# Optimization experiments

Measured on AMD Instinct MI355X. Metric: run time of the kernel, lower is better.

Reference implementation:

```python
import jax, jax.numpy as jnp
import numpy as np

KERNEL = 9


def setup_inputs() -> dict:
    key = jax.random.key(0)
    k1, k2 = jax.random.split(key)
    n, c, h, w = 1, 256, 256, 256
    key_feature = jax.random.normal(k1, (n, c, h, w), dtype=jnp.float32)
    weights = jax.random.normal(k2, (1, KERNEL * KERNEL, h, w), dtype=jnp.float32)
    return {"key_feature": key_feature, "weights": weights}


def reference(key_feature, weights):
    # Dynamic local filtering: out[n,c,y,x] = sum_{i,j} pad(key)[n,c,y+i,x+j] * weights[0, i*k+j, y, x]
    # Faithful to: img2col (unfold with zero pad) * per-pixel weights, summed over k^2.
    k = KERNEL
    p = k // 2
    n, c, h, w = key_feature.shape
    # weights.squeeze().view(k^2, -1): [k^2, h*w] -> here keep spatial layout [k^2, h, w]
    wk = weights.reshape(k * k, h, w)
    padded = jnp.pad(key_feature, ((0, 0), (0, 0), (p, p), (p, p)))
    out = jnp.zeros_like(key_feature)
    for i in range(k):
        for j in range(k):
            patch = padded[:, :, i:i + h, j:j + w]  # [n,c,h,w]
            out = out + patch * wk[i * k + j]       # broadcast [h,w] over [n,c]
    return out
```

## Files before the change

kernel.cpp:

```cpp
#include <hip/hip_runtime.h>

#define HH 256
#define WW 256
#define PAD 4
#define HW (HH * WW)

#define TW 32
#define TH 16
#define PR 24
#define PC 40
#define PCP 41
#define NSPLIT 4
#define CPB 64
#define NG 16
#define NSLOT 4

__device__ __forceinline__ void fma4(float4& a, const float4& k, float w) {
    a.x = fmaf(k.x, w, a.x);
    a.y = fmaf(k.y, w, a.y);
    a.z = fmaf(k.z, w, a.z);
    a.w = fmaf(k.w, w, a.w);
}

__global__ __launch_bounds__(256, 2)
void prop_kernel(const float* __restrict__ key, const float* __restrict__ wts,
                 float* __restrict__ out) {
    __shared__ float4 smem[2][PR][PCP];

    const int tid = threadIdx.x;
    const int tw  = tid & 15;
    const int th  = tid >> 4;
    const int w0  = blockIdx.x * TW;
    const int h0  = blockIdx.y * TH;
    const int c0  = blockIdx.z * CPB;
    const int h   = h0 + th;
    const int w   = w0 + 2 * tw;

    float wt0[81], wt1[81];
    {
        const float* wp = wts + h * WW + w;
        #pragma unroll
        for (int t = 0; t < 81; ++t) {
            float2 v = *reinterpret_cast<const float2*>(wp + t * HW);
            wt0[t] = v.x;
            wt1[t] = v.y;
        }
    }

    const float* sp[NSLOT];
    int  sdst[NSLOT];
    bool sin_[NSLOT];
    bool sact[NSLOT];
    #pragma unroll
    for (int k = 0; k < NSLOT; ++k) {
        int p   = tid + k * 256;
        bool act = p < PR * PC;
        int row = p / PC;
        int col = p - row * PC;
        int gh  = h0 - PAD + row;
        int gw  = w0 - PAD + col;
        bool inb = act && (unsigned)gh < HH && (unsigned)gw < WW;
        sact[k] = act;
        sin_[k] = inb;
        sdst[k] = row * PCP + col;
        sp[k]   = key + (size_t)c0 * HW + (inb ? (gh * WW + gw) : 0);
    }

    {
        float4 v[NSLOT];
        #pragma unroll
        for (int k = 0; k < NSLOT; ++k) {
            const float* q = sp[k];
            v[k].x = q[0];
            v[k].y = q[HW];
            v[k].z = q[2 * HW];
            v[k].w = q[3 * HW];
            if (!sin_[k]) v[k] = make_float4(0.f, 0.f, 0.f, 0.f);
            sp[k] += 4 * HW;
        }
        float4* dstb = &smem[0][0][0];
        #pragma unroll
        for (int k = 0; k < NSLOT; ++k)
            if (sact[k]) dstb[sdst[k]] = v[k];
    }
    __syncthreads();

    float* op = out + (size_t)c0 * HW + h * WW + w;

    for (int g = 0; g < NG; ++g) {
        const bool pf = (g + 1 < NG);

        float4 stg[NSLOT];
        if (pf) {
            #pragma unroll
            for (int k = 0; k < NSLOT; ++k) {
                const float* q = sp[k];
                stg[k].x = q[0];
                stg[k].y = q[HW];
                stg[k].z = q[2 * HW];
                stg[k].w = q[3 * HW];
                if (!sin_[k]) stg[k] = make_float4(0.f, 0.f, 0.f, 0.f);
                sp[k] += 4 * HW;
            }
        }

        const float4* bp = &smem[g & 1][0][0] + th * PCP + 2 * tw;
        float4 a0 = make_float4(0.f, 0.f, 0.f, 0.f);
        float4 a1 = make_float4(0.f, 0.f, 0.f, 0.f);
        #pragma unroll
        for (int r = 0; r < 9; ++r) {
            #pragma unroll
            for (int c = 0; c < 10; ++c) {
                float4 k4 = bp[r * PCP + c];
                if (c < 9)  fma4(a0, k4, wt0[r * 9 + c]);
                if (c >= 1) fma4(a1, k4, wt1[r * 9 + c - 1]);
            }
        }

        *reinterpret_cast<float2*>(op)          = make_float2(a0.x, a1.x);
        *reinterpret_cast<float2*>(op + HW)     = make_float2(a0.y, a1.y);
        *reinterpret_cast<float2*>(op + 2 * HW) = make_float2(a0.z, a1.z);
        *reinterpret_cast<float2*>(op + 3 * HW) = make_float2(a0.w, a1.w);
        op += 4 * HW;

        if (pf) {
            float4* dstb = &smem[(g + 1) & 1][0][0];
            #pragma unroll
            for (int k = 0; k < NSLOT; ++k)
                if (sact[k]) dstb[sdst[k]] = stg[k];
        }

        __syncthreads();
    }
}

extern "C" void kernel_launch(void* const* d_in, const int* in_sizes, int n_in,
                              void* d_out, int out_size, void* d_ws, size_t ws_size,
                              hipStream_t stream) {
    const float* key = (const float*)d_in[0];
    const float* wts = (const float*)d_in[1];
    float* out = (float*)d_out;

    dim3 grid(WW / TW, HH / TH, NSPLIT);
    prop_kernel<<<grid, 256, 0, stream>>>(key, wts, out);
}
```

Measured before the change: 196.2 us.

## Split filter taps across two thread halves to cut register use and raise occupancy

Each block now covers a smaller 8-row tile. Its 256 threads form two halves that each hold only half of the 81 per-pixel weights in registers. Each half computes partial sums over its tap range, and the second half passes its partials through shared memory so the first half can sum and store the result. The goal is to shrink the register footprint, allowing four blocks per CU instead of two. The cost is an extra barrier and shared-memory reduction per channel group, plus larger halo overhead relative to the smaller tile.

Result: slower. 294.6 us (+50.1%).

```diff
diff --git a/kernel.cpp b/kernel.cpp
--- a/kernel.cpp
+++ b/kernel.cpp
@@ -6,14 +6,14 @@
 #define HW (HH * WW)
 
 #define TW 32
-#define TH 16
-#define PR 24
+#define TH 8
+#define PR 16
 #define PC 40
 #define PCP 41
 #define NSPLIT 4
 #define CPB 64
 #define NG 16
-#define NSLOT 4
+#define NSLOT 3
 
 __device__ __forceinline__ void fma4(float4& a, const float4& k, float w) {
     a.x = fmaf(k.x, w, a.x);
@@ -22,28 +22,57 @@
     a.w = fmaf(k.w, w, a.w);
 }
 
-__global__ __launch_bounds__(256, 2)
+template<int LO, int HI>
+__device__ __forceinline__ void compute_taps(const float4* __restrict__ bp,
+                                             const float (&wt0)[41], const float (&wt1)[41],
+                                             float4& a0, float4& a1) {
+    #pragma unroll
+    for (int r = 0; r < 9; ++r) {
+        #pragma unroll
+        for (int c = 0; c < 10; ++c) {
+            constexpr int dummy = 0; (void)dummy;
+            const int t0 = r * 9 + c;
+            const int t1 = r * 9 + c - 1;
+            const bool u0 = (c < 9) && (t0 >= LO) && (t0 < HI);
+            const bool u1 = (c >= 1) && (t1 >= LO) && (t1 < HI);
+            if (u0 || u1) {
+                float4 k4 = bp[r * PCP + c];
+                if (u0) fma4(a0, k4, wt0[t0 - LO]);
+                if (u1) fma4(a1, k4, wt1[t1 - LO]);
+            }
+        }
+    }
+}
+
+__global__ __launch_bounds__(256, 4)
 void prop_kernel(const float* __restrict__ key, const float* __restrict__ wts,
                  float* __restrict__ out) {
-    __shared__ float4 smem[2][PR][PCP];
+    __shared__ float4 smem[2][PR * PCP];
+    __shared__ float4 red[128 * 3];
 
-    const int tid = threadIdx.x;
-    const int tw  = tid & 15;
-    const int th  = tid >> 4;
-    const int w0  = blockIdx.x * TW;
-    const int h0  = blockIdx.y * TH;
-    const int c0  = blockIdx.z * CPB;
-    const int h   = h0 + th;
-    const int w   = w0 + 2 * tw;
+    const int tid   = threadIdx.x;
+    const bool roleA = tid < 128;
+    const int q    = tid & 127;
+    const int tw   = q & 15;
+    const int th   = q >> 4;
+    const int w0   = blockIdx.x * TW;
+    const int h0   = blockIdx.y * TH;
+    const int c0   = blockIdx.z * CPB;
+    const int h    = h0 + th;
+    const int w    = w0 + 2 * tw;
 
-    float wt0[81], wt1[81];
+    float wt0[41], wt1[41];
     {
-        const float* wp = wts + h * WW + w;
+        const int lo  = roleA ? 0 : 41;
+        const int cnt = roleA ? 41 : 40;
+        const float* wp = wts + (size_t)lo * HW + h * WW + w;
         #pragma unroll
-        for (int t = 0; t < 81; ++t) {
-            float2 v = *reinterpret_cast<const float2*>(wp + t * HW);
-            wt0[t] = v.x;
-            wt1[t] = v.y;
+        for (int t = 0; t < 41; ++t) {
+            if (t < cnt) {
+                float2 v = *reinterpret_cast<const float2*>(wp + (size_t)t * HW);
+                wt0[t] = v.x;
+                wt1[t] = v.y;
+            }
         }
     }
 
@@ -70,18 +99,17 @@
         float4 v[NSLOT];
         #pragma unroll
         for (int k = 0; k < NSLOT; ++k) {
-            const float* q = sp[k];
-            v[k].x = q[0];
-            v[k].y = q[HW];
-            v[k].z = q[2 * HW];
-            v[k].w = q[3 * HW];
+            const float* qp = sp[k];
+            v[k].x = qp[0];
+            v[k].y = qp[HW];
+            v[k].z = qp[2 * HW];
+            v[k].w = qp[3 * HW];
             if (!sin_[k]) v[k] = make_float4(0.f, 0.f, 0.f, 0.f);
             sp[k] += 4 * HW;
         }
-        float4* dstb = &smem[0][0][0];
         #pragma unroll
         for (int k = 0; k < NSLOT; ++k)
-            if (sact[k]) dstb[sdst[k]] = v[k];
+            if (sact[k]) smem[0][sdst[k]] = v[k];
     }
     __syncthreads();
 
@@ -94,40 +122,44 @@
         if (pf) {
             #pragma unroll
             for (int k = 0; k < NSLOT; ++k) {
-                const float* q = sp[k];
-                stg[k].x = q[0];
-                stg[k].y = q[HW];
-                stg[k].z = q[2 * HW];
-                stg[k].w = q[3 * HW];
+                const float* qp = sp[k];
+                stg[k].x = qp[0];
+                stg[k].y = qp[HW];
+                stg[k].z = qp[2 * HW];
+                stg[k].w = qp[3 * HW];
                 if (!sin_[k]) stg[k] = make_float4(0.f, 0.f, 0.f, 0.f);
                 sp[k] += 4 * HW;
             }
         }
 
-        const float4* bp = &smem[g & 1][0][0] + th * PCP + 2 * tw;
+        const float4* bp = &smem[g & 1][th * PCP + 2 * tw];
         float4 a0 = make_float4(0.f, 0.f, 0.f, 0.f);
         float4 a1 = make_float4(0.f, 0.f, 0.f, 0.f);
-        #pragma unroll
-        for (int r = 0; r < 9; ++r) {
-            #pragma unroll
-            for (int c = 0; c < 10; ++c) {
-                float4 k4 = bp[r * PCP + c];
-                if (c < 9)  fma4(a0, k4, wt0[r * 9 + c]);
-                if (c >= 1) fma4(a1, k4, wt1[r * 9 + c - 1]);
-            }
+        if (roleA) compute_taps<0, 41>(bp, wt0, wt1, a0, a1);
+        else       compute_taps<41, 81>(bp, wt0, wt1, a0, a1);
+
+        if (!roleA) {
+            red[q * 3]     = a0;
+            red[q * 3 + 1] = a1;
         }
+        __syncthreads();
 
-        *reinterpret_cast<float2*>(op)          = make_float2(a0.x, a1.x);
-        *reinterpret_cast<float2*>(op + HW)     = make_float2(a0.y, a1.y);
-        *reinterpret_cast<float2*>(op + 2 * HW) = make_float2(a0.z, a1.z);
-        *reinterpret_cast<float2*>(op + 3 * HW) = make_float2(a0.w, a1.w);
+        if (roleA) {
+            float4 b0 = red[q * 3];
+            float4 b1 = red[q * 3 + 1];
+            a0.x += b0.x; a0.y += b0.y; a0.z += b0.z; a0.w += b0.w;
+            a1.x += b1.x; a1.y += b1.y; a1.z += b1.z; a1.w += b1.w;
+            *reinterpret_cast<float2*>(op)          = make_float2(a0.x, a1.x);
+            *reinterpret_cast<float2*>(op + HW)     = make_float2(a0.y, a1.y);
+            *reinterpret_cast<float2*>(op + 2 * HW) = make_float2(a0.z, a1.z);
+            *reinterpret_cast<float2*>(op + 3 * HW) = make_float2(a0.w, a1.w);
+        }
         op += 4 * HW;
 
         if (pf) {
-            float4* dstb = &smem[(g + 1) & 1][0][0];
             #pragma unroll
             for (int k = 0; k < NSLOT; ++k)
-                if (sact[k]) dstb[sdst[k]] = stg[k];
+                if (sact[k]) smem[(g + 1) & 1][sdst[k]] = stg[k];
         }
 
         __syncthreads();
```

## Split 9x9 filter into two row-half passes to cut registers and raise occupancy

Applied to the files above, without the earlier changes.

The kernel is split into two launches. Each handles about half of the 81 filter taps: the first pass covers rows 0-3 plus half of row 4, and the second covers the rest of row 4 plus rows 5-8. The second pass accumulates into the output written by the first. This shrinks per-thread weight registers and the shared tile, so launch bounds go up to 4 blocks per SM, and the channel split doubles to 8. The cost is a second read of the input halo rows, a read-modify-write of the whole output, and an extra kernel launch.

Result: slower. 437.9 us (+123.2%).

```diff
diff --git a/kernel.cpp b/kernel.cpp
--- a/kernel.cpp
+++ b/kernel.cpp
@@ -7,13 +7,16 @@
 
 #define TW 32
 #define TH 16
-#define PR 24
+#define PR 20
 #define PC 40
 #define PCP 41
-#define NSPLIT 4
-#define CPB 64
-#define NG 16
+#define NSPLIT 8
+#define CPB 32
+#define NG 8
 #define NSLOT 4
+
+__host__ __device__ constexpr int clo_f(int PASS, int lr) { return (PASS == 1 && lr == 0) ? 5 : 0; }
+__host__ __device__ constexpr int chi_f(int PASS, int lr) { return (PASS == 0 && lr == 4) ? 5 : 9; }
 
 __device__ __forceinline__ void fma4(float4& a, const float4& k, float w) {
     a.x = fmaf(k.x, w, a.x);
@@ -22,10 +25,11 @@
     a.w = fmaf(k.w, w, a.w);
 }
 
-__global__ __launch_bounds__(256, 2)
-void prop_kernel(const float* __restrict__ key, const float* __restrict__ wts,
-                 float* __restrict__ out) {
-    __shared__ float4 smem[2][PR][PCP];
+template<int PASS>
+__global__ __launch_bounds__(256, 4)
+void prop_pass(const float* __restrict__ key, const float* __restrict__ wts,
+               float* __restrict__ out) {
+    __shared__ float4 smem[2][PR * PCP];
 
     const int tid = threadIdx.x;
     const int tw  = tid & 15;
@@ -36,29 +40,36 @@
     const int h   = h0 + th;
     const int w   = w0 + 2 * tw;
 
-    float wt0[81], wt1[81];
+    float wt0[5][9], wt1[5][9];
     {
         const float* wp = wts + h * WW + w;
         #pragma unroll
-        for (int t = 0; t < 81; ++t) {
-            float2 v = *reinterpret_cast<const float2*>(wp + t * HW);
-            wt0[t] = v.x;
-            wt1[t] = v.y;
+        for (int lr = 0; lr < 5; ++lr) {
+            #pragma unroll
+            for (int c = 0; c < 9; ++c) {
+                if (c >= clo_f(PASS, lr) && c < chi_f(PASS, lr)) {
+                    const int t = (lr + 4 * PASS) * 9 + c;
+                    float2 v = *reinterpret_cast<const float2*>(wp + (size_t)t * HW);
+                    wt0[lr][c] = v.x;
+                    wt1[lr][c] = v.y;
+                }
+            }
         }
     }
 
+    const int gh0 = h0 - 4 * (1 - PASS);
     const float* sp[NSLOT];
     int  sdst[NSLOT];
     bool sin_[NSLOT];
     bool sact[NSLOT];
     #pragma unroll
     for (int k = 0; k < NSLOT; ++k) {
-        int p   = tid + k * 256;
+        int p    = tid + k * 256;
         bool act = p < PR * PC;
-        int row = p / PC;
-        int col = p - row * PC;
-        int gh  = h0 - PAD + row;
-        int gw  = w0 - PAD + col;
+        int row  = p / PC;
+        int col  = p - row * PC;
+        int gh   = gh0 + row;
+        int gw   = w0 - PAD + col;
         bool inb = act && (unsigned)gh < HH && (unsigned)gw < WW;
         sact[k] = act;
         sin_[k] = inb;
@@ -78,10 +89,9 @@
             if (!sin_[k]) v[k] = make_float4(0.f, 0.f, 0.f, 0.f);
             sp[k] += 4 * HW;
         }
-        float4* dstb = &smem[0][0][0];
         #pragma unroll
         for (int k = 0; k < NSLOT; ++k)
-            if (sact[k]) dstb[sdst[k]] = v[k];
+            if (sact[k]) smem[0][sdst[k]] = v[k];
     }
     __syncthreads();
 
@@ -104,30 +114,46 @@
             }
         }
 
-        const float4* bp = &smem[g & 1][0][0] + th * PCP + 2 * tw;
+        const float4* bp = &smem[g & 1][th * PCP + 2 * tw];
         float4 a0 = make_float4(0.f, 0.f, 0.f, 0.f);
         float4 a1 = make_float4(0.f, 0.f, 0.f, 0.f);
         #pragma unroll
-        for (int r = 0; r < 9; ++r) {
+        for (int lr = 0; lr < 5; ++lr) {
             #pragma unroll
-            for (int c = 0; c < 10; ++c) {
-                float4 k4 = bp[r * PCP + c];
-                if (c < 9)  fma4(a0, k4, wt0[r * 9 + c]);
-                if (c >= 1) fma4(a1, k4, wt1[r * 9 + c - 1]);
+            for (int cc = 0; cc <= 9; ++cc) {
+                const int cl = clo_f(PASS, lr);
+                const int ch = chi_f(PASS, lr);
+                const bool u0 = (cc >= cl) && (cc < ch);
+                const bool u1 = (cc - 1 >= cl) && (cc - 1 < ch);
+                if (u0 || u1) {
+                    float4 k4 = bp[lr * PCP + cc];
+                    if (u0) fma4(a0, k4, wt0[lr][cc]);
+                    if (u1) fma4(a1, k4, wt1[lr][cc - 1]);
+                }
             }
         }
 
-        *reinterpret_cast<float2*>(op)          = make_float2(a0.x, a1.x);
-        *reinterpret_cast<float2*>(op + HW)     = make_float2(a0.y, a1.y);
-        *reinterpret_cast<float2*>(op + 2 * HW) = make_float2(a0.z, a1.z);
-        *reinterpret_cast<float2*>(op + 3 * HW) = make_float2(a0.w, a1.w);
+        if (PASS == 0) {
+            *reinterpret_cast<float2*>(op)          = make_float2(a0.x, a1.x);
+            *reinterpret_cast<float2*>(op + HW)     = make_float2(a0.y, a1.y);
+            *reinterpret_cast<float2*>(op + 2 * HW) = make_float2(a0.z, a1.z);
+            *reinterpret_cast<float2*>(op + 3 * HW) = make_float2(a0.w, a1.w);
+        } else {
+            float2 o0 = *reinterpret_cast<float2*>(op);
+            float2 o1 = *reinterpret_cast<float2*>(op + HW);
+            float2 o2 = *reinterpret_cast<float2*>(op + 2 * HW);
+            float2 o3 = *reinterpret_cast<float2*>(op + 3 * HW);
+            *reinterpret_cast<float2*>(op)          = make_float2(o0.x + a0.x, o0.y + a1.x);
+            *reinterpret_cast<float2*>(op + HW)     = make_float2(o1.x + a0.y, o1.y + a1.y);
+            *reinterpret_cast<float2*>(op + 2 * HW) = make_float2(o2.x + a0.z, o2.y + a1.z);
+            *reinterpret_cast<float2*>(op + 3 * HW) = make_float2(o3.x + a0.w, o3.y + a1.w);
+        }
         op += 4 * HW;
 
         if (pf) {
-            float4* dstb = &smem[(g + 1) & 1][0][0];
             #pragma unroll
             for (int k = 0; k < NSLOT; ++k)
-                if (sact[k]) dstb[sdst[k]] = stg[k];
+                if (sact[k]) smem[(g + 1) & 1][sdst[k]] = stg[k];
         }
 
         __syncthreads();
@@ -142,5 +168,6 @@
     float* out = (float*)d_out;
 
     dim3 grid(WW / TW, HH / TH, NSPLIT);
-    prop_kernel<<<grid, 256, 0, stream>>>(key, wts, out);
+    prop_pass<0><<<grid, 256, 0, stream>>>(key, wts, out);
+    prop_pass<1><<<grid, 256, 0, stream>>>(key, wts, out);
 }
```
